# Performance work log

Hardware: AMD Instinct MI355X
Metric: run time of the kernel (lower is better)

The kernel has to match this reference:

```python
import jax, jax.numpy as jnp
import numpy as np

N_EMBD, D_INNER, DT_RANK, D_CONV, D_STATE, SEQ_LEN = 2048, 4096, 128, 4, 16, 2048


def setup_inputs() -> dict:
    key = jax.random.key(0)
    ks = jax.random.split(key, 8)
    sc = lambda fan_in: 1.0 / np.sqrt(fan_in)
    x = jax.random.normal(ks[0], (SEQ_LEN, N_EMBD), dtype=jnp.float32)
    in_proj_w = jax.random.normal(ks[1], (2 * D_INNER, N_EMBD), jnp.float32) * sc(N_EMBD)
    in_proj_b = jnp.zeros((2 * D_INNER,), jnp.float32)
    conv_w = jax.random.normal(ks[2], (D_INNER, 1, D_CONV), jnp.float32) * sc(D_CONV)
    conv_b = jnp.zeros((D_INNER,), jnp.float32)
    ssm_in_w = jax.random.normal(ks[3], (DT_RANK + 2 * D_STATE, D_INNER), jnp.float32) * sc(D_INNER)
    delta_w = jax.random.normal(ks[4], (D_INNER, DT_RANK), jnp.float32) * sc(DT_RANK)
    # A_log init exactly as module: repeat(arange(1,d_state+1), d_inner).reshape(d_inner,d_state)
    A_log = jnp.log(jnp.repeat(jnp.arange(1, D_STATE + 1), D_INNER).reshape(D_INNER, D_STATE).astype(jnp.float32))
    D = jnp.ones((D_INNER,), jnp.float32)
    out_w = jax.random.normal(ks[5], (N_EMBD, D_INNER), jnp.float32) * sc(D_INNER)
    out_b = jnp.zeros((N_EMBD,), jnp.float32)
    return {"x": x, "in_proj_w": in_proj_w, "in_proj_b": in_proj_b, "conv_w": conv_w,
            "conv_b": conv_b, "ssm_in_w": ssm_in_w, "delta_w": delta_w, "A_log": A_log,
            "D": D, "out_w": out_w, "out_b": out_b}


def selective_scan(u, delta, A, B, C, D):
    # u, delta: (L, di); A: (di, ds); B, C: (L, ds); D: (di,)
    dA = jnp.exp(delta[:, :, None] * A[None, :, :])                # (L, di, ds)
    dBu = delta[:, :, None] * B[:, None, :] * u[:, :, None]        # (L, di, ds)

    def step(h, inp):
        dA_t, dBu_t, C_t = inp
        h = dA_t * h + dBu_t                                       # (di, ds)
        y = jnp.einsum('ds,s->d', h, C_t)
        return h, y

    h0 = jnp.zeros((u.shape[1], A.shape[1]), u.dtype)
    _, ys = jax.lax.scan(step, h0, (dA, dBu, C))
    return ys + u * D                                              # (L, di)


def mamba_block(x, in_proj_w, in_proj_b, conv_w, conv_b, ssm_in_w, delta_w, A_log, D, out_w, out_b):
    L = x.shape[0]
    xr = x @ in_proj_w.T + in_proj_b                               # (L, 2*di)
    xi, res = jnp.split(xr, 2, axis=-1)
    # depthwise causal conv1d: left-pad d_conv-1 (== first L outputs of symmetric pad)
    xc = jax.lax.conv_general_dilated(
        xi.T[None],                                                # (1, di, L)
        conv_w,                                                    # (di, 1, k)
        window_strides=(1,), padding=[(D_CONV - 1, 0)],
        feature_group_count=D_INNER)[0] + conv_b[:, None]
    xc = jax.nn.silu(xc.T)                                         # (L, di)
    # SSM
    A = -jnp.exp(A_log)
    dbc = xc @ ssm_in_w.T                                          # (L, dt_rank + 2*ds)
    delta, B, C = jnp.split(dbc, [DT_RANK, DT_RANK + D_STATE], axis=-1)
    delta = jax.nn.softplus(delta @ delta_w.T)                     # (L, di)
    y = selective_scan(xc, delta, A, B, C, D)
    y = y * jax.nn.silu(res)
    return y @ out_w.T + out_b                                     # (L, n_embd)


def reference(x, in_proj_w, in_proj_b, conv_w, conv_b, ssm_in_w, delta_w, A_log, D, out_w, out_b):
    return mamba_block(x, in_proj_w, in_proj_b, conv_w, conv_b, ssm_in_w, delta_w, A_log, D, out_w, out_b)
```

## Files before the change

### kernel.cpp

```cpp
#include <hip/hip_runtime.h>
#include <cstdint>
#include <cstddef>


typedef __bf16 bf16x8 __attribute__((ext_vector_type(8)));
typedef float f32x4 __attribute__((ext_vector_type(4)));

#define GLDS16(g, l)                                        \
  __builtin_amdgcn_global_load_lds(                         \
      (__attribute__((address_space(1))) void*)(g),         \
      (__attribute__((address_space(3))) void*)(l), 16, 0, 0)

#define FENCE() asm volatile("" ::: "memory")
#define BARRIER()                      \
  do {                                 \
    FENCE();                           \
    __builtin_amdgcn_s_barrier();      \
    FENCE();                           \
  } while (0)

static __device__ __forceinline__ unsigned short f2b(float f) {
  unsigned int x = __builtin_bit_cast(unsigned int, f);
  x += 0x7fffu + ((x >> 16) & 1u);
  return (unsigned short)(x >> 16);
}

static __device__ __forceinline__ float sigmoidf_fast(float x) {
  return 1.0f / (1.0f + __expf(-x));
}

__global__ __launch_bounds__(256) void cast_f32_bf16(
    const float* __restrict__ src, unsigned short* __restrict__ dst, int n4) {
  int stride = gridDim.x * 256;
  for (int i = blockIdx.x * 256 + threadIdx.x; i < n4; i += stride) {
    float4 v = reinterpret_cast<const float4*>(src)[i];
    ushort4 o;
    o.x = f2b(v.x); o.y = f2b(v.y); o.z = f2b(v.z); o.w = f2b(v.w);
    reinterpret_cast<ushort4*>(dst)[i] = o;
  }
}

template <int MODE>
__global__ __launch_bounds__(512) void gemm256_bt(
    const unsigned short* __restrict__ A, const unsigned short* __restrict__ B,
    float* __restrict__ C, const float* __restrict__ bias,
    int M, int N, int K, int Kslice) {
  __shared__ __align__(16) unsigned short lds[65536];
  const int tid = threadIdx.x;
  const int l = tid & 63;
  const int w = tid >> 6;
  const int wr = w >> 2;
  const int wc = w & 3;

  const int nwg = gridDim.x * gridDim.y;
  const int q = nwg >> 3;
  int flat = blockIdx.x + gridDim.x * blockIdx.y;
  flat = (flat & 7) * q + (flat >> 3);
  const int bx = flat % gridDim.x;
  const int by = flat / gridDim.x;

  const long brow = (long)bx * 256;
  const long bcol = (long)by * 256;
  const int ks = blockIdx.z;
  const int NT = Kslice >> 6;

  f32x4 acc[8][4] = {};

  const unsigned short* Ab = A + (size_t)brow * K + (size_t)ks * Kslice;
  const unsigned short* Bb = B + (size_t)bcol * K + (size_t)ks * Kslice;
  size_t soff[4];
  int doff[4];
#pragma unroll
  for (int i = 0; i < 4; ++i) {
    int idx = i * 512 + tid;
    int r = idx >> 3, s = idx & 7;
    soff[i] = (size_t)r * K + (size_t)((s ^ (r & 7)) << 3);
    doff[i] = idx * 8;
  }

  auto stage = [&](int kt, int buf) {
    const int k0 = kt << 6;
#pragma unroll
    for (int i = 0; i < 4; ++i)
      GLDS16(Ab + soff[i] + k0, &lds[buf * 32768 + doff[i]]);
#pragma unroll
    for (int i = 0; i < 4; ++i)
      GLDS16(Bb + soff[i] + k0, &lds[buf * 32768 + 16384 + doff[i]]);
  };

  const int hi = l >> 4, lo7 = l & 7;
  const int sw0 = ((0 + hi) ^ lo7) << 3;
  const int sw1 = ((4 + hi) ^ lo7) << 3;
  const int rowA = wr * 128 + (l & 15);
  const int colB = wc * 64 + (l & 15);

  stage(0, 0);
  stage(1, 1);

  int buf = 0;
  for (int kt = 0; kt < NT; ++kt) {
    const bool last = (kt == NT - 1);
    if (last) {
      asm volatile("s_waitcnt vmcnt(0)" ::: "memory");
    } else {
      asm volatile("s_waitcnt vmcnt(8)" ::: "memory");
    }
    BARRIER();
    const int bb = buf * 32768;
    bf16x8 a0[8], b0[4];
#pragma unroll
    for (int m = 0; m < 8; ++m)
      a0[m] = *reinterpret_cast<const bf16x8*>(&lds[bb + (rowA + m * 16) * 64 + sw0]);
#pragma unroll
    for (int n = 0; n < 4; ++n)
      b0[n] = *reinterpret_cast<const bf16x8*>(&lds[bb + 16384 + (colB + n * 16) * 64 + sw0]);
    __builtin_amdgcn_s_setprio(1);
#pragma unroll
    for (int m = 0; m < 8; ++m)
#pragma unroll
      for (int n = 0; n < 4; ++n)
        acc[m][n] = __builtin_amdgcn_mfma_f32_16x16x32_bf16(a0[m], b0[n], acc[m][n], 0, 0, 0);
    __builtin_amdgcn_s_setprio(0);
    bf16x8 a1[8], b1[4];
#pragma unroll
    for (int m = 0; m < 8; ++m)
      a1[m] = *reinterpret_cast<const bf16x8*>(&lds[bb + (rowA + m * 16) * 64 + sw1]);
#pragma unroll
    for (int n = 0; n < 4; ++n)
      b1[n] = *reinterpret_cast<const bf16x8*>(&lds[bb + 16384 + (colB + n * 16) * 64 + sw1]);
    asm volatile("s_waitcnt lgkmcnt(0)" ::: "memory");
    __builtin_amdgcn_sched_barrier(0);
    BARRIER();
    if (kt + 2 < NT) stage(kt + 2, buf);
    __builtin_amdgcn_s_setprio(1);
#pragma unroll
    for (int m = 0; m < 8; ++m)
#pragma unroll
      for (int n = 0; n < 4; ++n)
        acc[m][n] = __builtin_amdgcn_mfma_f32_16x16x32_bf16(a1[m], b1[n], acc[m][n], 0, 0, 0);
    __builtin_amdgcn_s_setprio(0);
    buf ^= 1;
  }

  const long r0 = brow + wr * 128 + (l >> 4) * 4;
  const long c0 = bcol + wc * 64 + (l & 15);
  float* Cb = (MODE == 1) ? C + (size_t)ks * M * N : C;
#pragma unroll
  for (int m = 0; m < 8; ++m) {
#pragma unroll
    for (int n = 0; n < 4; ++n) {
      long col = c0 + n * 16;
      float bv = (MODE == 0) ? bias[col] : 0.0f;
#pragma unroll
      for (int r = 0; r < 4; ++r)
        Cb[(r0 + m * 16 + r) * (long)N + col] = acc[m][n][r] + bv;
    }
  }
}

__global__ __launch_bounds__(256) void reduce4_bias(
    const float* __restrict__ part, const float* __restrict__ bias,
    float* __restrict__ out, int n4) {
  int stride = gridDim.x * 256;
  for (int f = blockIdx.x * 256 + threadIdx.x; f < n4; f += stride) {
    float4 s0 = reinterpret_cast<const float4*>(part)[f];
    float4 s1 = reinterpret_cast<const float4*>(part + 4194304ull)[f];
    float4 s2 = reinterpret_cast<const float4*>(part + 8388608ull)[f];
    float4 s3 = reinterpret_cast<const float4*>(part + 12582912ull)[f];
    float4 bv = reinterpret_cast<const float4*>(bias)[f & 511];
    float4 o;
    o.x = s0.x + s1.x + s2.x + s3.x + bv.x;
    o.y = s0.y + s1.y + s2.y + s3.y + bv.y;
    o.z = s0.z + s1.z + s2.z + s3.z + bv.z;
    o.w = s0.w + s1.w + s2.w + s3.w + bv.w;
    reinterpret_cast<float4*>(out)[f] = o;
  }
}

template <int EPI>
__global__ __launch_bounds__(256) void gemm_bt(
    const unsigned short* __restrict__ A, const unsigned short* __restrict__ B,
    float* __restrict__ C, const float* __restrict__ bias,
    int M, int N, int K) {
  __shared__ __align__(16) unsigned short lA[128 * 32];
  __shared__ __align__(16) unsigned short lB[128 * 32];
  const int tid = threadIdx.x;
  const int l = tid & 63;
  const int w = tid >> 6;
  const int wr = w >> 1, wc = w & 1;
  const long brow = (long)blockIdx.x * 128;
  const long bcol = (long)blockIdx.y * 128;

  f32x4 acc[4][4] = {};

  const int srow = tid >> 2;
  const int scol = (tid & 3) * 8;

  const unsigned short* Ab = A + (size_t)brow * K;
  const unsigned short* Bb = B + (size_t)bcol * K;

  for (int k0 = 0; k0 < K; k0 += 32) {
#pragma unroll
    for (int j = 0; j < 2; ++j) {
      GLDS16(Ab + (size_t)(j * 64 + srow) * K + k0 + scol, &lA[j * 2048 + tid * 8]);
      GLDS16(Bb + (size_t)(j * 64 + srow) * K + k0 + scol, &lB[j * 2048 + tid * 8]);
    }
    __syncthreads();
    bf16x8 af[4], bfr[4];
#pragma unroll
    for (int mt = 0; mt < 4; ++mt)
      af[mt] = *reinterpret_cast<const bf16x8*>(
          &lA[(wr * 64 + mt * 16 + (l & 15)) * 32 + (l >> 4) * 8]);
#pragma unroll
    for (int nt = 0; nt < 4; ++nt)
      bfr[nt] = *reinterpret_cast<const bf16x8*>(
          &lB[(wc * 64 + nt * 16 + (l & 15)) * 32 + (l >> 4) * 8]);
#pragma unroll
    for (int mt = 0; mt < 4; ++mt)
#pragma unroll
      for (int nt = 0; nt < 4; ++nt)
        acc[mt][nt] = __builtin_amdgcn_mfma_f32_16x16x32_bf16(
            af[mt], bfr[nt], acc[mt][nt], 0, 0, 0);
    __syncthreads();
  }

  const long r0 = brow + wr * 64 + ((l >> 4) * 4);
  const long c0 = bcol + wc * 64 + (l & 15);
#pragma unroll
  for (int mt = 0; mt < 4; ++mt) {
#pragma unroll
    for (int nt = 0; nt < 4; ++nt) {
      long col = c0 + nt * 16;
      float bv = (EPI == 0) ? bias[col] : 0.0f;
#pragma unroll
      for (int r = 0; r < 4; ++r) {
        long row = r0 + mt * 16 + r;
        float v = acc[mt][nt][r] + bv;
        if (EPI == 1) v = (v > 20.0f) ? v : log1pf(__expf(v));
        C[row * (long)N + col] = v;
      }
    }
  }
}

__global__ __launch_bounds__(256) void conv_silu_k(
    const float* __restrict__ xr, const float* __restrict__ cw,
    const float* __restrict__ cb, float* __restrict__ xc,
    unsigned short* __restrict__ xcb) {
  const int d = blockIdx.x * 256 + threadIdx.x;
  const int t0 = blockIdx.y * 128;
  const float4 wv = *reinterpret_cast<const float4*>(cw + (size_t)d * 4);
  const float bv = cb[d];
  float xm3 = (t0 >= 3) ? xr[(size_t)(t0 - 3) * 8192 + d] : 0.0f;
  float xm2 = (t0 >= 2) ? xr[(size_t)(t0 - 2) * 8192 + d] : 0.0f;
  float xm1 = (t0 >= 1) ? xr[(size_t)(t0 - 1) * 8192 + d] : 0.0f;
  for (int tt = 0; tt < 128; ++tt) {
    const size_t t = (size_t)t0 + tt;
    float xt = xr[t * 8192 + d];
    float a = bv + wv.x * xm3 + wv.y * xm2 + wv.z * xm1 + wv.w * xt;
    float s = a * sigmoidf_fast(a);
    xc[t * 4096 + d] = s;
    xcb[t * 4096 + d] = f2b(s);
    xm3 = xm2; xm2 = xm1; xm1 = xt;
  }
}

__global__ __launch_bounds__(256) void gemm_dbc(
    const unsigned short* __restrict__ A, const unsigned short* __restrict__ B,
    float* __restrict__ part) {
  __shared__ __align__(16) unsigned short lA[64 * 32];
  __shared__ __align__(16) unsigned short lB[160 * 32];
  const int tid = threadIdx.x;
  const int l = tid & 63, w = tid >> 6;
  const int brow = blockIdx.x * 64;
  const int ks = blockIdx.y;
  const int K = 4096;
  f32x4 acc[10] = {};
  const int srow = tid >> 2, scol = (tid & 3) * 8;
  for (int k0 = ks * 512; k0 < ks * 512 + 512; k0 += 32) {
    GLDS16(A + (size_t)(brow + srow) * K + k0 + scol, &lA[tid * 8]);
#pragma unroll
    for (int j = 0; j < 3; ++j) {
      int li = j * 256 + tid;
      if (li < 640) {
        GLDS16(B + (size_t)(li >> 2) * K + k0 + (li & 3) * 8, &lB[li * 8]);
      }
    }
    __syncthreads();
    bf16x8 af = *reinterpret_cast<const bf16x8*>(
        &lA[(w * 16 + (l & 15)) * 32 + (l >> 4) * 8]);
#pragma unroll
    for (int nt = 0; nt < 10; ++nt) {
      bf16x8 bfr = *reinterpret_cast<const bf16x8*>(
          &lB[(nt * 16 + (l & 15)) * 32 + (l >> 4) * 8]);
      acc[nt] = __builtin_amdgcn_mfma_f32_16x16x32_bf16(af, bfr, acc[nt], 0, 0, 0);
    }
    __syncthreads();
  }
  const int r0 = brow + w * 16 + (l >> 4) * 4;
  const int c = l & 15;
#pragma unroll
  for (int nt = 0; nt < 10; ++nt)
#pragma unroll
    for (int r = 0; r < 4; ++r)
      part[((size_t)ks * 2048 + r0 + r) * 160 + nt * 16 + c] = acc[nt][r];
}

__global__ __launch_bounds__(256) void reduce_dbc(
    const float* __restrict__ part, unsigned short* __restrict__ drb,
    float* __restrict__ bc) {
  int idx = blockIdx.x * 256 + threadIdx.x;
  float s = 0.0f;
#pragma unroll
  for (int k = 0; k < 8; ++k) s += part[(size_t)k * 2048 * 160 + idx];
  int row = idx / 160, col = idx - row * 160;
  if (col < 128) drb[row * 128 + col] = f2b(s);
  else bc[row * 32 + (col - 128)] = s;
}

__global__ __launch_bounds__(256) void scan_passA(
    const float* __restrict__ delta, const float* __restrict__ xc,
    const float* __restrict__ bc, const float* __restrict__ alog,
    float* __restrict__ P, float* __restrict__ S) {
  __shared__ float lbc[1024];
  const int d = blockIdx.x * 256 + threadIdx.x;
  const int c = blockIdx.y;
  const int t0 = c * 32;
#pragma unroll
  for (int j = 0; j < 4; ++j) {
    int idx = j * 256 + threadIdx.x;
    lbc[idx] = bc[(size_t)t0 * 32 + idx];
  }
  __syncthreads();
  float a[16], h[16], p[16];
#pragma unroll
  for (int s = 0; s < 16; ++s) {
    a[s] = -__expf(alog[(size_t)d * 16 + s]);
    h[s] = 0.0f;
    p[s] = 1.0f;
  }
  for (int tt = 0; tt < 32; ++tt) {
    float dt = delta[(size_t)(t0 + tt) * 4096 + d];
    float u = xc[(size_t)(t0 + tt) * 4096 + d];
    float du = dt * u;
#pragma unroll
    for (int s = 0; s < 16; ++s) {
      float e = __expf(dt * a[s]);
      h[s] = e * h[s] + du * lbc[tt * 32 + s];
      p[s] *= e;
    }
  }
  size_t o = ((size_t)c * 4096 + d) * 16;
#pragma unroll
  for (int s = 0; s < 16; s += 4) {
    *reinterpret_cast<float4*>(&P[o + s]) = make_float4(p[s], p[s + 1], p[s + 2], p[s + 3]);
    *reinterpret_cast<float4*>(&S[o + s]) = make_float4(h[s], h[s + 1], h[s + 2], h[s + 3]);
  }
}

__global__ __launch_bounds__(256) void scan_passB(
    float* __restrict__ P, const float* __restrict__ S) {
  const int idx = blockIdx.x * 256 + threadIdx.x;
  float h = 0.0f;
  for (int c = 0; c < 64; ++c) {
    size_t o = (size_t)c * 65536 + idx;
    float p = P[o], sv = S[o];
    P[o] = h;
    h = p * h + sv;
  }
}

__global__ __launch_bounds__(256) void scan_passC(
    const float* __restrict__ delta, const float* __restrict__ xc,
    const float* __restrict__ bc, const float* __restrict__ alog,
    const float* __restrict__ hst, const float* __restrict__ Dp,
    const float* __restrict__ xr, unsigned short* __restrict__ yb) {
  __shared__ float lbc[1024];
  const int d = blockIdx.x * 256 + threadIdx.x;
  const int c = blockIdx.y;
  const int t0 = c * 32;
#pragma unroll
  for (int j = 0; j < 4; ++j) {
    int idx = j * 256 + threadIdx.x;
    lbc[idx] = bc[(size_t)t0 * 32 + idx];
  }
  __syncthreads();
  float a[16], h[16];
  size_t o = ((size_t)c * 4096 + d) * 16;
#pragma unroll
  for (int s = 0; s < 16; ++s) {
    a[s] = -__expf(alog[(size_t)d * 16 + s]);
    h[s] = hst[o + s];
  }
  const float Dv = Dp[d];
  for (int tt = 0; tt < 32; ++tt) {
    float dt = delta[(size_t)(t0 + tt) * 4096 + d];
    float u = xc[(size_t)(t0 + tt) * 4096 + d];
    float du = dt * u;
    float y = 0.0f;
#pragma unroll
    for (int s = 0; s < 16; ++s) {
      float e = __expf(dt * a[s]);
      h[s] = e * h[s] + du * lbc[tt * 32 + s];
      y += h[s] * lbc[tt * 32 + 16 + s];
    }
    float res = xr[(size_t)(t0 + tt) * 8192 + 4096 + d];
    float v = (y + u * Dv) * (res * sigmoidf_fast(res));
    yb[(size_t)(t0 + tt) * 4096 + d] = f2b(v);
  }
}

extern "C" void kernel_launch(void* const* d_in, const int* in_sizes, int n_in,
                              void* d_out, int out_size, void* d_ws, size_t ws_size,
                              hipStream_t stream) {
  const float* x    = (const float*)d_in[0];
  const float* w1   = (const float*)d_in[1];
  const float* b1   = (const float*)d_in[2];
  const float* cw   = (const float*)d_in[3];
  const float* cb   = (const float*)d_in[4];
  const float* w2   = (const float*)d_in[5];
  const float* w3   = (const float*)d_in[6];
  const float* alog = (const float*)d_in[7];
  const float* Dp   = (const float*)d_in[8];
  const float* w4   = (const float*)d_in[9];
  const float* b4   = (const float*)d_in[10];
  float* out = (float*)d_out;

  char* ws = (char*)d_ws;
  size_t off = 0;
  auto alloc = [&](size_t b) {
    size_t o = off;
    off += (b + 255) & ~(size_t)255;
    return o;
  };
  unsigned short* w1b = (unsigned short*)(ws + alloc(2ull * 8192 * 2048));
  unsigned short* xb  = (unsigned short*)(ws + alloc(2ull * 2048 * 2048));
  unsigned short* w2b = (unsigned short*)(ws + alloc(2ull * 160 * 4096));
  unsigned short* w3b = (unsigned short*)(ws + alloc(2ull * 4096 * 128));
  unsigned short* w4b = (unsigned short*)(ws + alloc(2ull * 2048 * 4096));
  float* xr   = (float*)(ws + alloc(4ull * 2048 * 8192));
  float* xc   = (float*)(ws + alloc(4ull * 2048 * 4096));
  unsigned short* xcb = (unsigned short*)(ws + alloc(2ull * 2048 * 4096));
  unsigned short* drb = (unsigned short*)(ws + alloc(2ull * 2048 * 128));
  float* bcb  = (float*)(ws + alloc(4ull * 2048 * 32));
  float* delta = (float*)(ws + alloc(4ull * 2048 * 4096));
  float* part = delta;
  float* P = (float*)(ws + alloc(4ull * 64 * 4096 * 16));
  float* S = (float*)(ws + alloc(4ull * 64 * 4096 * 16));
  unsigned short* yb = (unsigned short*)S;
  float* part4 = xr;

  if (ws_size < off) return;

  cast_f32_bf16<<<2048, 256, 0, stream>>>(w1, w1b, 8192 * 2048 / 4);
  cast_f32_bf16<<<1024, 256, 0, stream>>>(x, xb, 2048 * 2048 / 4);
  cast_f32_bf16<<<640, 256, 0, stream>>>(w2, w2b, 160 * 4096 / 4);
  cast_f32_bf16<<<512, 256, 0, stream>>>(w3, w3b, 4096 * 128 / 4);
  cast_f32_bf16<<<2048, 256, 0, stream>>>(w4, w4b, 2048 * 4096 / 4);

  gemm256_bt<0><<<dim3(8, 32, 1), 512, 0, stream>>>(xb, w1b, xr, b1, 2048, 8192, 2048, 2048);
  conv_silu_k<<<dim3(16, 16), 256, 0, stream>>>(xr, cw, cb, xc, xcb);
  gemm_dbc<<<dim3(32, 8), 256, 0, stream>>>(xcb, w2b, part);
  reduce_dbc<<<1280, 256, 0, stream>>>(part, drb, bcb);
  gemm_bt<1><<<dim3(16, 32), 256, 0, stream>>>(drb, w3b, delta, nullptr, 2048, 4096, 128);
  scan_passA<<<dim3(16, 64), 256, 0, stream>>>(delta, xc, bcb, alog, P, S);
  scan_passB<<<256, 256, 0, stream>>>(P, S);
  scan_passC<<<dim3(16, 64), 256, 0, stream>>>(delta, xc, bcb, alog, P, Dp, xr, yb);
  gemm256_bt<1><<<dim3(8, 8, 4), 512, 0, stream>>>(yb, w4b, part4, nullptr, 2048, 2048, 4096, 1024);
  reduce4_bias<<<1024, 256, 0, stream>>>(part4, b4, out, 2048 * 2048 / 4);
}
```

Measured before the change: 331.8 us.

## Switch GEMM mainloop to BK=32 with 4-slot ring buffer, 3-deep prefetch

The bf16 GEMM mainloop now moves K in 32-wide tiles instead of 64-wide ones. It uses a 4-slot LDS ring with three tiles prefetched ahead, in place of the old 2-buffer double buffering, and the LDS swizzle is changed to match the 64-byte rows. The next stage is issued right after the barrier, and each iteration splits its MFMAs into two halves so the second half of the A fragments loads after the first batch. The aim is deeper latency hiding for the global loads and fewer registers held per tile. The cost is twice as many iterations and barriers per K, which adds synchronisation overhead.

```diff
diff --git a/kernel.cpp b/kernel.cpp
--- a/kernel.cpp
+++ b/kernel.cpp
@@ -62,84 +62,85 @@
   const long brow = (long)bx * 256;
   const long bcol = (long)by * 256;
   const int ks = blockIdx.z;
-  const int NT = Kslice >> 6;
+  const int NT = Kslice >> 5;
 
   f32x4 acc[8][4] = {};
 
   const unsigned short* Ab = A + (size_t)brow * K + (size_t)ks * Kslice;
   const unsigned short* Bb = B + (size_t)bcol * K + (size_t)ks * Kslice;
-  size_t soff[4];
-  int doff[4];
-#pragma unroll
-  for (int i = 0; i < 4; ++i) {
+
+  size_t soff[2];
+  int doff[2];
+#pragma unroll
+  for (int i = 0; i < 2; ++i) {
     int idx = i * 512 + tid;
-    int r = idx >> 3, s = idx & 7;
-    soff[i] = (size_t)r * K + (size_t)((s ^ (r & 7)) << 3);
+    int r = idx >> 2, p = idx & 3;
+    soff[i] = (size_t)r * K + (size_t)((p ^ ((r >> 1) & 3)) << 3);
     doff[i] = idx * 8;
   }
 
-  auto stage = [&](int kt, int buf) {
-    const int k0 = kt << 6;
-#pragma unroll
-    for (int i = 0; i < 4; ++i)
-      GLDS16(Ab + soff[i] + k0, &lds[buf * 32768 + doff[i]]);
-#pragma unroll
-    for (int i = 0; i < 4; ++i)
-      GLDS16(Bb + soff[i] + k0, &lds[buf * 32768 + 16384 + doff[i]]);
+  auto stage = [&](int kt) {
+    const int slot = (kt & 3) * 16384;
+    const int k0 = kt << 5;
+#pragma unroll
+    for (int i = 0; i < 2; ++i)
+      GLDS16(Ab + soff[i] + k0, &lds[slot + doff[i]]);
+#pragma unroll
+    for (int i = 0; i < 2; ++i)
+      GLDS16(Bb + soff[i] + k0, &lds[slot + 8192 + doff[i]]);
   };
 
-  const int hi = l >> 4, lo7 = l & 7;
-  const int sw0 = ((0 + hi) ^ lo7) << 3;
-  const int sw1 = ((4 + hi) ^ lo7) << 3;
-  const int rowA = wr * 128 + (l & 15);
-  const int colB = wc * 64 + (l & 15);
-
-  stage(0, 0);
-  stage(1, 1);
-
-  int buf = 0;
+  const int la = l & 15, hi = l >> 4;
+  const int sw = (hi ^ ((la >> 1) & 3)) * 8;
+  const int aoff = (wr * 128 + la) * 32 + sw;
+  const int boff = 8192 + (wc * 64 + la) * 32 + sw;
+
+  stage(0);
+  if (NT > 1) stage(1);
+  if (NT > 2) stage(2);
+
   for (int kt = 0; kt < NT; ++kt) {
-    const bool last = (kt == NT - 1);
-    if (last) {
-      asm volatile("s_waitcnt vmcnt(0)" ::: "memory");
-    } else {
-      asm volatile("s_waitcnt vmcnt(8)" ::: "memory");
-    }
+    const int rem = NT - 1 - kt;
+    if (rem >= 2)      asm volatile("s_waitcnt vmcnt(8)" ::: "memory");
+    else if (rem == 1) asm volatile("s_waitcnt vmcnt(4)" ::: "memory");
+    else               asm volatile("s_waitcnt vmcnt(0)" ::: "memory");
     BARRIER();
-    const int bb = buf * 32768;
-    bf16x8 a0[8], b0[4];
-#pragma unroll
-    for (int m = 0; m < 8; ++m)
-      a0[m] = *reinterpret_cast<const bf16x8*>(&lds[bb + (rowA + m * 16) * 64 + sw0]);
-#pragma unroll
-    for (int n = 0; n < 4; ++n)
-      b0[n] = *reinterpret_cast<const bf16x8*>(&lds[bb + 16384 + (colB + n * 16) * 64 + sw0]);
-    __builtin_amdgcn_s_setprio(1);
-#pragma unroll
-    for (int m = 0; m < 8; ++m)
-#pragma unroll
-      for (int n = 0; n < 4; ++n)
-        acc[m][n] = __builtin_amdgcn_mfma_f32_16x16x32_bf16(a0[m], b0[n], acc[m][n], 0, 0, 0);
-    __builtin_amdgcn_s_setprio(0);
-    bf16x8 a1[8], b1[4];
-#pragma unroll
-    for (int m = 0; m < 8; ++m)
-      a1[m] = *reinterpret_cast<const bf16x8*>(&lds[bb + (rowA + m * 16) * 64 + sw1]);
-#pragma unroll
-    for (int n = 0; n < 4; ++n)
-      b1[n] = *reinterpret_cast<const bf16x8*>(&lds[bb + 16384 + (colB + n * 16) * 64 + sw1]);
+    if (kt + 3 < NT) stage(kt + 3);
+    const int sb = (kt & 3) * 16384;
+
+    bf16x8 av[4], bv[4];
+#pragma unroll
+    for (int mt = 0; mt < 4; ++mt)
+      av[mt] = *reinterpret_cast<const bf16x8*>(&lds[sb + aoff + mt * 512]);
+#pragma unroll
+    for (int nt = 0; nt < 4; ++nt)
+      bv[nt] = *reinterpret_cast<const bf16x8*>(&lds[sb + boff + nt * 512]);
     asm volatile("s_waitcnt lgkmcnt(0)" ::: "memory");
     __builtin_amdgcn_sched_barrier(0);
+    __builtin_amdgcn_s_setprio(1);
+#pragma unroll
+    for (int mt = 0; mt < 4; ++mt)
+#pragma unroll
+      for (int nt = 0; nt < 4; ++nt)
+        acc[mt][nt] = __builtin_amdgcn_mfma_f32_16x16x32_bf16(av[mt], bv[nt], acc[mt][nt], 0, 0, 0);
+    __builtin_amdgcn_s_setprio(0);
+    __builtin_amdgcn_sched_barrier(0);
     BARRIER();
-    if (kt + 2 < NT) stage(kt + 2, buf);
+
+    bf16x8 av2[4];
+#pragma unroll
+    for (int mt = 0; mt < 4; ++mt)
+      av2[mt] = *reinterpret_cast<const bf16x8*>(&lds[sb + aoff + (mt + 4) * 512]);
+    asm volatile("s_waitcnt lgkmcnt(0)" ::: "memory");
+    __builtin_amdgcn_sched_barrier(0);
     __builtin_amdgcn_s_setprio(1);
 #pragma unroll
-    for (int m = 0; m < 8; ++m)
-#pragma unroll
-      for (int n = 0; n < 4; ++n)
-        acc[m][n] = __builtin_amdgcn_mfma_f32_16x16x32_bf16(a1[m], b1[n], acc[m][n], 0, 0, 0);
+    for (int mt = 0; mt < 4; ++mt)
+#pragma unroll
+      for (int nt = 0; nt < 4; ++nt)
+        acc[mt + 4][nt] = __builtin_amdgcn_mfma_f32_16x16x32_bf16(av2[mt], bv[nt], acc[mt + 4][nt], 0, 0, 0);
     __builtin_amdgcn_s_setprio(0);
-    buf ^= 1;
+    __builtin_amdgcn_sched_barrier(0);
   }
 
   const long r0 = brow + wr * 128 + (l >> 4) * 4;
@@ -150,10 +151,10 @@
 #pragma unroll
     for (int n = 0; n < 4; ++n) {
       long col = c0 + n * 16;
-      float bv = (MODE == 0) ? bias[col] : 0.0f;
+      float bvx = (MODE == 0) ? bias[col] : 0.0f;
 #pragma unroll
       for (int r = 0; r < 4; ++r)
-        Cb[(r0 + m * 16 + r) * (long)N + col] = acc[m][n][r] + bv;
+        Cb[(r0 + m * 16 + r) * (long)N + col] = acc[m][n][r] + bvx;
     }
   }
 }
```

Result: no change. 338.2 us (+1.9%).

## Emit bf16 intermediates from in_proj epilogue, fuse silu(res), merge cast launches

Applied to the files above, without the earlier changes.

The in_proj GEMM epilogue now writes its two halves as bf16 buffers, one holding xi and one holding silu(res), instead of a float32 xr buffer. The conv, scan pass A and scan pass C kernels then read bf16 inputs, and the float32 xc copy is dropped. This cuts global memory traffic for the large intermediates and removes the sigmoid work from the scan. The five weight/input cast launches are merged into one kernel. The cost is bf16 rounding of xi, u and the gate, which adds numerical error.

```diff
diff --git a/kernel.cpp b/kernel.cpp
--- a/kernel.cpp
+++ b/kernel.cpp
@@ -25,25 +25,42 @@
   return (unsigned short)(x >> 16);
 }
 
+static __device__ __forceinline__ float b2f(unsigned short u) {
+  return __builtin_bit_cast(float, (unsigned int)u << 16);
+}
+
 static __device__ __forceinline__ float sigmoidf_fast(float x) {
   return 1.0f / (1.0f + __expf(-x));
 }
 
-__global__ __launch_bounds__(256) void cast_f32_bf16(
-    const float* __restrict__ src, unsigned short* __restrict__ dst, int n4) {
-  int stride = gridDim.x * 256;
-  for (int i = blockIdx.x * 256 + threadIdx.x; i < n4; i += stride) {
-    float4 v = reinterpret_cast<const float4*>(src)[i];
-    ushort4 o;
-    o.x = f2b(v.x); o.y = f2b(v.y); o.z = f2b(v.z); o.w = f2b(v.w);
-    reinterpret_cast<ushort4*>(dst)[i] = o;
+struct CastArgs {
+  const float* src[5];
+  unsigned short* dst[5];
+  int n4[5];
+};
+
+__global__ __launch_bounds__(256) void cast_multi(CastArgs a) {
+  const int stride = gridDim.x * 256;
+  const int t = blockIdx.x * 256 + threadIdx.x;
+#pragma unroll
+  for (int k = 0; k < 5; ++k) {
+    const float4* src = reinterpret_cast<const float4*>(a.src[k]);
+    ushort4* dst = reinterpret_cast<ushort4*>(a.dst[k]);
+    const int n4 = a.n4[k];
+    for (int i = t; i < n4; i += stride) {
+      float4 v = src[i];
+      ushort4 o;
+      o.x = f2b(v.x); o.y = f2b(v.y); o.z = f2b(v.z); o.w = f2b(v.w);
+      dst[i] = o;
+    }
   }
 }
 
 template <int MODE>
 __global__ __launch_bounds__(512) void gemm256_bt(
     const unsigned short* __restrict__ A, const unsigned short* __restrict__ B,
-    float* __restrict__ C, const float* __restrict__ bias,
+    float* __restrict__ Cp, unsigned short* __restrict__ xib,
+    unsigned short* __restrict__ rsb, const float* __restrict__ bias,
     int M, int N, int K, int Kslice) {
   __shared__ __align__(16) unsigned short lds[65536];
   const int tid = threadIdx.x;
@@ -144,17 +161,37 @@
 
   const long r0 = brow + wr * 128 + (l >> 4) * 4;
   const long c0 = bcol + wc * 64 + (l & 15);
-  float* Cb = (MODE == 1) ? C + (size_t)ks * M * N : C;
-#pragma unroll
-  for (int m = 0; m < 8; ++m) {
-#pragma unroll
-    for (int n = 0; n < 4; ++n) {
-      long col = c0 + n * 16;
-      float bv = (MODE == 0) ? bias[col] : 0.0f;
-#pragma unroll
-      for (int r = 0; r < 4; ++r)
-        Cb[(r0 + m * 16 + r) * (long)N + col] = acc[m][n][r] + bv;
-    }
+  if (MODE == 1) {
+    float* Cb = Cp + (size_t)ks * M * N;
+#pragma unroll
+    for (int m = 0; m < 8; ++m)
+#pragma unroll
+      for (int n = 0; n < 4; ++n) {
+        long col = c0 + n * 16;
+#pragma unroll
+        for (int r = 0; r < 4; ++r)
+          Cb[(r0 + m * 16 + r) * (long)N + col] = acc[m][n][r];
+      }
+  } else {
+#pragma unroll
+    for (int m = 0; m < 8; ++m)
+#pragma unroll
+      for (int n = 0; n < 4; ++n) {
+        long col = c0 + n * 16;
+        float bv = bias[col];
+        const bool isres = col >= 4096;
+        long cc = isres ? col - 4096 : col;
+#pragma unroll
+        for (int r = 0; r < 4; ++r) {
+          float v = acc[m][n][r] + bv;
+          if (isres) {
+            float s = v * sigmoidf_fast(v);
+            rsb[(r0 + m * 16 + r) * 4096 + cc] = f2b(s);
+          } else {
+            xib[(r0 + m * 16 + r) * 4096 + cc] = f2b(v);
+          }
+        }
+      }
   }
 }
 
@@ -177,11 +214,9 @@
   }
 }
 
-template <int EPI>
-__global__ __launch_bounds__(256) void gemm_bt(
+__global__ __launch_bounds__(256) void gemm_bt_sp(
     const unsigned short* __restrict__ A, const unsigned short* __restrict__ B,
-    float* __restrict__ C, const float* __restrict__ bias,
-    int M, int N, int K) {
+    float* __restrict__ C, int M, int N, int K) {
   __shared__ __align__(16) unsigned short lA[128 * 32];
   __shared__ __align__(16) unsigned short lB[128 * 32];
   const int tid = threadIdx.x;
@@ -231,12 +266,11 @@
 #pragma unroll
     for (int nt = 0; nt < 4; ++nt) {
       long col = c0 + nt * 16;
-      float bv = (EPI == 0) ? bias[col] : 0.0f;
 #pragma unroll
       for (int r = 0; r < 4; ++r) {
         long row = r0 + mt * 16 + r;
-        float v = acc[mt][nt][r] + bv;
-        if (EPI == 1) v = (v > 20.0f) ? v : log1pf(__expf(v));
+        float v = acc[mt][nt][r];
+        v = (v > 20.0f) ? v : log1pf(__expf(v));
         C[row * (long)N + col] = v;
       }
     }
@@ -244,22 +278,20 @@
 }
 
 __global__ __launch_bounds__(256) void conv_silu_k(
-    const float* __restrict__ xr, const float* __restrict__ cw,
-    const float* __restrict__ cb, float* __restrict__ xc,
-    unsigned short* __restrict__ xcb) {
+    const unsigned short* __restrict__ xib, const float* __restrict__ cw,
+    const float* __restrict__ cb, unsigned short* __restrict__ xcb) {
   const int d = blockIdx.x * 256 + threadIdx.x;
   const int t0 = blockIdx.y * 128;
   const float4 wv = *reinterpret_cast<const float4*>(cw + (size_t)d * 4);
   const float bv = cb[d];
-  float xm3 = (t0 >= 3) ? xr[(size_t)(t0 - 3) * 8192 + d] : 0.0f;
-  float xm2 = (t0 >= 2) ? xr[(size_t)(t0 - 2) * 8192 + d] : 0.0f;
-  float xm1 = (t0 >= 1) ? xr[(size_t)(t0 - 1) * 8192 + d] : 0.0f;
+  float xm3 = (t0 >= 3) ? b2f(xib[(size_t)(t0 - 3) * 4096 + d]) : 0.0f;
+  float xm2 = (t0 >= 2) ? b2f(xib[(size_t)(t0 - 2) * 4096 + d]) : 0.0f;
+  float xm1 = (t0 >= 1) ? b2f(xib[(size_t)(t0 - 1) * 4096 + d]) : 0.0f;
   for (int tt = 0; tt < 128; ++tt) {
     const size_t t = (size_t)t0 + tt;
-    float xt = xr[t * 8192 + d];
+    float xt = b2f(xib[t * 4096 + d]);
     float a = bv + wv.x * xm3 + wv.y * xm2 + wv.z * xm1 + wv.w * xt;
     float s = a * sigmoidf_fast(a);
-    xc[t * 4096 + d] = s;
     xcb[t * 4096 + d] = f2b(s);
     xm3 = xm2; xm2 = xm1; xm1 = xt;
   }
@@ -319,7 +351,7 @@
 }
 
 __global__ __launch_bounds__(256) void scan_passA(
-    const float* __restrict__ delta, const float* __restrict__ xc,
+    const float* __restrict__ delta, const unsigned short* __restrict__ xcb,
     const float* __restrict__ bc, const float* __restrict__ alog,
     float* __restrict__ P, float* __restrict__ S) {
   __shared__ float lbc[1024];
@@ -341,7 +373,7 @@
   }
   for (int tt = 0; tt < 32; ++tt) {
     float dt = delta[(size_t)(t0 + tt) * 4096 + d];
-    float u = xc[(size_t)(t0 + tt) * 4096 + d];
+    float u = b2f(xcb[(size_t)(t0 + tt) * 4096 + d]);
     float du = dt * u;
 #pragma unroll
     for (int s = 0; s < 16; ++s) {
@@ -371,10 +403,10 @@
 }
 
 __global__ __launch_bounds__(256) void scan_passC(
-    const float* __restrict__ delta, const float* __restrict__ xc,
+    const float* __restrict__ delta, const unsigned short* __restrict__ xcb,
     const float* __restrict__ bc, const float* __restrict__ alog,
     const float* __restrict__ hst, const float* __restrict__ Dp,
-    const float* __restrict__ xr, unsigned short* __restrict__ yb) {
+    const unsigned short* __restrict__ rsb, unsigned short* __restrict__ yb) {
   __shared__ float lbc[1024];
   const int d = blockIdx.x * 256 + threadIdx.x;
   const int c = blockIdx.y;
@@ -395,7 +427,7 @@
   const float Dv = Dp[d];
   for (int tt = 0; tt < 32; ++tt) {
     float dt = delta[(size_t)(t0 + tt) * 4096 + d];
-    float u = xc[(size_t)(t0 + tt) * 4096 + d];
+    float u = b2f(xcb[(size_t)(t0 + tt) * 4096 + d]);
     float du = dt * u;
     float y = 0.0f;
 #pragma unroll
@@ -404,8 +436,8 @@
       h[s] = e * h[s] + du * lbc[tt * 32 + s];
       y += h[s] * lbc[tt * 32 + 16 + s];
     }
-    float res = xr[(size_t)(t0 + tt) * 8192 + 4096 + d];
-    float v = (y + u * Dv) * (res * sigmoidf_fast(res));
+    float rs = b2f(rsb[(size_t)(t0 + tt) * 4096 + d]);
+    float v = (y + u * Dv) * rs;
     yb[(size_t)(t0 + tt) * 4096 + d] = f2b(v);
   }
 }
@@ -438,34 +470,38 @@
   unsigned short* w2b = (unsigned short*)(ws + alloc(2ull * 160 * 4096));
   unsigned short* w3b = (unsigned short*)(ws + alloc(2ull * 4096 * 128));
   unsigned short* w4b = (unsigned short*)(ws + alloc(2ull * 2048 * 4096));
-  float* xr   = (float*)(ws + alloc(4ull * 2048 * 8192));
-  float* xc   = (float*)(ws + alloc(4ull * 2048 * 4096));
+  unsigned short* xib = (unsigned short*)(ws + alloc(2ull * 2048 * 4096));
+  unsigned short* rsb = (unsigned short*)(ws + alloc(2ull * 2048 * 4096));
   unsigned short* xcb = (unsigned short*)(ws + alloc(2ull * 2048 * 4096));
   unsigned short* drb = (unsigned short*)(ws + alloc(2ull * 2048 * 128));
   float* bcb  = (float*)(ws + alloc(4ull * 2048 * 32));
   float* delta = (float*)(ws + alloc(4ull * 2048 * 4096));
-  float* part = delta;
   float* P = (float*)(ws + alloc(4ull * 64 * 4096 * 16));
   float* S = (float*)(ws + alloc(4ull * 64 * 4096 * 16));
-  unsigned short* yb = (unsigned short*)S;
-  float* part4 = xr;
+  float* part  = delta;
+  unsigned short* yb = xib;
+  float* part4 = delta;
 
   if (ws_size < off) return;
 
-  cast_f32_bf16<<<2048, 256, 0, stream>>>(w1, w1b, 8192 * 2048 / 4);
-  cast_f32_bf16<<<1024, 256, 0, stream>>>(x, xb, 2048 * 2048 / 4);
-  cast_f32_bf16<<<640, 256, 0, stream>>>(w2, w2b, 160 * 4096 / 4);
-  cast_f32_bf16<<<512, 256, 0, stream>>>(w3, w3b, 4096 * 128 / 4);
-  cast_f32_bf16<<<2048, 256, 0, stream>>>(w4, w4b, 2048 * 4096 / 4);
-
-  gemm256_bt<0><<<dim3(8, 32, 1), 512, 0, stream>>>(xb, w1b, xr, b1, 2048, 8192, 2048, 2048);
-  conv_silu_k<<<dim3(16, 16), 256, 0, stream>>>(xr, cw, cb, xc, xcb);
+  CastArgs ca;
+  ca.src[0] = w1; ca.dst[0] = w1b; ca.n4[0] = 8192 * 2048 / 4;
+  ca.src[1] = x;  ca.dst[1] = xb;  ca.n4[1] = 2048 * 2048 / 4;
+  ca.src[2] = w2; ca.dst[2] = w2b; ca.n4[2] = 160 * 4096 / 4;
+  ca.src[3] = w3; ca.dst[3] = w3b; ca.n4[3] = 4096 * 128 / 4;
+  ca.src[4] = w4; ca.dst[4] = w4b; ca.n4[4] = 2048 * 4096 / 4;
+  cast_multi<<<2048, 256, 0, stream>>>(ca);
+
+  gemm256_bt<2><<<dim3(8, 32, 1), 512, 0, stream>>>(
+      xb, w1b, nullptr, xib, rsb, b1, 2048, 8192, 2048, 2048);
+  conv_silu_k<<<dim3(16, 16), 256, 0, stream>>>(xib, cw, cb, xcb);
   gemm_dbc<<<dim3(32, 8), 256, 0, stream>>>(xcb, w2b, part);
   reduce_dbc<<<1280, 256, 0, stream>>>(part, drb, bcb);
-  gemm_bt<1><<<dim3(16, 32), 256, 0, stream>>>(drb, w3b, delta, nullptr, 2048, 4096, 128);
-  scan_passA<<<dim3(16, 64), 256, 0, stream>>>(delta, xc, bcb, alog, P, S);
+  gemm_bt_sp<<<dim3(16, 32), 256, 0, stream>>>(drb, w3b, delta, 2048, 4096, 128);
+  scan_passA<<<dim3(16, 64), 256, 0, stream>>>(delta, xcb, bcb, alog, P, S);
   scan_passB<<<256, 256, 0, stream>>>(P, S);
-  scan_passC<<<dim3(16, 64), 256, 0, stream>>>(delta, xc, bcb, alog, P, Dp, xr, yb);
-  gemm256_bt<1><<<dim3(8, 8, 4), 512, 0, stream>>>(yb, w4b, part4, nullptr, 2048, 2048, 4096, 1024);
+  scan_passC<<<dim3(16, 64), 256, 0, stream>>>(delta, xcb, bcb, alog, P, Dp, rsb, yb);
+  gemm256_bt<1><<<dim3(8, 8, 4), 512, 0, stream>>>(
+      yb, w4b, part4, nullptr, nullptr, nullptr, 2048, 2048, 4096, 1024);
   reduce4_bias<<<1024, 256, 0, stream>>>(part4, b4, out, 2048 * 2048 / 4);
 }
```

Result: faster. 315.2 us (-5.0%).
